# Optimization experiments

Measured on AMD Instinct MI355X. Metric: run time of the kernel, lower is better.

The kernel has to match this reference:

```python
import jax, jax.numpy as jnp
import numpy as np
import math

B, E, H, HD, P, G, N, L, FF = 16, 768, 12, 64, 16, 14, 196, 12, 3072
SQRT_E = math.sqrt(E)
SQRT_HD = math.sqrt(HD)


def cosine_norm(x):
    n = jnp.linalg.norm(x, axis=-1, keepdims=True)
    return x / jnp.maximum(n, 1e-6)


def layer_norm(x, w, b, eps=1e-6):
    m = jnp.mean(x, axis=-1, keepdims=True)
    v = jnp.var(x, axis=-1, keepdims=True)
    return (x - m) / jnp.sqrt(v + eps) * w + b


def setup_inputs() -> dict:
    key = jax.random.key(0)
    ks = jax.random.split(key, 16)
    std = 0.02
    return {
        "x": jax.random.normal(ks[0], (B, 3, 224, 224), jnp.float32),
        "patch_w": jax.random.normal(ks[1], (E, 3, P, P), jnp.float32) * std,
        "patch_b": jnp.zeros((E,), jnp.float32),
        "cls_token": jax.random.normal(ks[2], (1, 1, E), jnp.float32) * std,
        "pos_embed": jax.random.normal(ks[3], (1, N + 1, E), jnp.float32) * std,
        "Wq": jax.random.normal(ks[4], (L, E, E), jnp.float32) * std,
        "Wk": jax.random.normal(ks[5], (L, E, E), jnp.float32) * std,
        "Wv": jax.random.normal(ks[6], (L, E, E), jnp.float32) * std,
        "Wo": jax.random.normal(ks[7], (L, E, E), jnp.float32) * std,
        # Scale params stored at their torch init values (s = ones * scale)
        "s_qk": jnp.ones((L, H, HD), jnp.float32) / SQRT_E,        # scale=1/sqrt(dim)
        "Wup": jax.random.normal(ks[8], (L, FF, E), jnp.float32) * std,
        "Wgate": jax.random.normal(ks[9], (L, FF, E), jnp.float32) * std,
        "Wdown": jax.random.normal(ks[10], (L, E, FF), jnp.float32) * std,
        "s_u": jnp.ones((L, FF), jnp.float32),
        "s_v": jnp.ones((L, FF), jnp.float32),
        "alpha_A": jnp.ones((L, E), jnp.float32) / SQRT_E,         # scale=1/sqrt(dim)
        "alpha_M": jnp.ones((L, E), jnp.float32) / SQRT_E,
        "fc_w": jnp.ones((E,), jnp.float32),
        "fc_b": jnp.zeros((E,), jnp.float32),
    }


def _attention(h, wq, wk, wv, wo, s_qk):
    b, n, _ = h.shape
    q = (h @ wq.T).reshape(b, n, H, HD)
    k = (h @ wk.T).reshape(b, n, H, HD)
    v = (h @ wv.T).reshape(b, n, H, HD)
    # Scale.forward(): s * (init/scale) with init=1, scale=1/sqrt(E)
    s = s_qk * SQRT_E                                   # [H, HD]
    q = cosine_norm(q) * s
    k = cosine_norm(k) * s
    logits = jnp.einsum("bnhd,bmhd->bhnm", q, k) * SQRT_HD
    attn = jax.nn.softmax(logits, axis=-1)
    out = jnp.einsum("bhnm,bmhd->bnhd", attn, v).reshape(b, n, E)
    return out @ wo.T


def _mlp(h, wup, wgate, wdown, s_u, s_v):
    u = (h @ wup.T) * s_u
    v = (h @ wgate.T) * s_v * SQRT_E                    # mlp scale = sqrt(in_features)
    hidden = u * jax.nn.silu(v)
    return hidden @ wdown.T


def _block(h, wq, wk, wv, wo, s_qk, wup, wgate, wdown, s_u, s_v, a_A, a_M):
    # alpha Scale: init=0.05, scale=1/sqrt(E) -> effective = s * 0.05 * sqrt(E)
    aA = a_A * (0.05 * SQRT_E)
    aM = a_M * (0.05 * SQRT_E)
    h_A = cosine_norm(_attention(h, wq, wk, wv, wo, s_qk))
    h = cosine_norm(h + aA * (h_A - h))
    h_M = cosine_norm(_mlp(h, wup, wgate, wdown, s_u, s_v))
    h = cosine_norm(h + aM * (h_M - h))
    return h


def reference(x, patch_w, patch_b, cls_token, pos_embed, Wq, Wk, Wv, Wo, s_qk,
              Wup, Wgate, Wdown, s_u, s_v, alpha_A, alpha_M, fc_w, fc_b):
    b = x.shape[0]
    # patch embed: conv k=stride=16 == patch extraction + linear proj
    patches = x.reshape(b, 3, G, P, G, P).transpose(0, 2, 4, 1, 3, 5).reshape(b, N, 3 * P * P)
    t = patches @ patch_w.reshape(E, -1).T + patch_b    # [B, N, E]
    t = jnp.concatenate([jnp.broadcast_to(cls_token, (b, 1, E)), t], axis=1)
    t = t + pos_embed                                    # [B, N+1, E]
    nodes = None
    for i in range(L):
        t = _block(t, Wq[i], Wk[i], Wv[i], Wo[i], s_qk[i],
                   Wup[i], Wgate[i], Wdown[i], s_u[i], s_v[i], alpha_A[i], alpha_M[i])
        if i == L - 2:
            nodes = layer_norm(t, fc_w, fc_b)[:, 1:]
    edges = layer_norm(t, fc_w, fc_b)[:, 1:]
    return nodes, edges
```

## Files before the change

### kernel.cpp

```cpp
#include <hip/hip_runtime.h>
#include <hip/hip_bf16.h>
#include <cstdint>
#include <cstddef>

typedef __hip_bfloat16 bf16;
typedef short bf16x8 __attribute__((ext_vector_type(8)));
typedef float f32x4 __attribute__((ext_vector_type(4)));

#define SQRT_E   27.712812921102035f
#define ASCALE   (0.05f * 27.712812921102035f)
#define MPAD     3200

__device__ __forceinline__ void load_lds16(const bf16* g, bf16* l) {
    __builtin_amdgcn_global_load_lds(
        (const __attribute__((address_space(1))) void*)g,
        (__attribute__((address_space(3))) void*)l, 16, 0, 0);
}

__device__ __forceinline__ float block_sum(float v, float* sbuf) {
#pragma unroll
    for (int m = 32; m >= 1; m >>= 1) v += __shfl_xor(v, m);
    __syncthreads();
    if ((threadIdx.x & 63) == 0) sbuf[threadIdx.x >> 6] = v;
    __syncthreads();
    return sbuf[0] + sbuf[1] + sbuf[2] + sbuf[3];
}

__device__ __forceinline__ void cvt8(const float* s, bf16* d) {
    float4 f0 = *(const float4*)s;
    float4 f1 = *(const float4*)(s + 4);
    bf16 t[8];
    t[0] = __float2bfloat16(f0.x); t[1] = __float2bfloat16(f0.y);
    t[2] = __float2bfloat16(f0.z); t[3] = __float2bfloat16(f0.w);
    t[4] = __float2bfloat16(f1.x); t[5] = __float2bfloat16(f1.y);
    t[6] = __float2bfloat16(f1.z); t[7] = __float2bfloat16(f1.w);
    *reinterpret_cast<uint4*>(d) = *reinterpret_cast<const uint4*>(t);
}

__device__ __forceinline__ void wconv_body(
    int idx,
    const float* __restrict__ wq, const float* __restrict__ wk,
    const float* __restrict__ wv, const float* __restrict__ wo,
    const float* __restrict__ wu, const float* __restrict__ wg,
    const float* __restrict__ wd, bf16* __restrict__ dst) {
    const float* src;
    size_t off;
    if (idx < 294912) {
        int seg = idx / 73728, o = idx - seg * 73728;
        src = (seg == 0) ? wq : (seg == 1) ? wk : (seg == 2) ? wv : wo;
        off = (size_t)o * 8;
    } else {
        int i2 = idx - 294912;
        int seg = i2 / 294912, o = i2 - seg * 294912;
        src = (seg == 0) ? wu : (seg == 1) ? wg : wd;
        off = (size_t)o * 8;
    }
    cvt8(src + off, dst + (size_t)idx * 8);
}

__global__ __launch_bounds__(256) void prep_kernel(
    const float* __restrict__ x, bf16* __restrict__ A,
    const float* __restrict__ patchw, bf16* __restrict__ pwb,
    const float* __restrict__ wq, const float* __restrict__ wk,
    const float* __restrict__ wv, const float* __restrict__ wo,
    const float* __restrict__ wu, const float* __restrict__ wg,
    const float* __restrict__ wd, bf16* __restrict__ wdst) {
    int b = blockIdx.x, tid = threadIdx.x;
    if (b < 288) {
        int idx = b * 256 + tid;
        cvt8(patchw + (size_t)idx * 8, pwb + (size_t)idx * 8);
    } else if (b < 9888) {
        int idx = (b - 288) * 256 + tid;
        int row = idx / 768, col = idx - row * 768;
        if (row >= 3136) { A[idx] = __float2bfloat16(0.f); return; }
        int bb = row / 196, pp = row - bb * 196;
        int gy = pp / 14, gx = pp - gy * 14;
        int c = col >> 8, rem = col & 255, py = rem >> 4, px = rem & 15;
        A[idx] = __float2bfloat16(
            x[((size_t)(bb * 3 + c) * 224 + gy * 16 + py) * 224 + gx * 16 + px]);
    } else {
        int idx = (b - 9888) * 256 + tid;
        wconv_body(idx, wq, wk, wv, wo, wu, wg, wd, wdst);
    }
}

__global__ __launch_bounds__(256) void assemble_kernel(
    const float* __restrict__ tproj, const float* __restrict__ pb,
    const float* __restrict__ cls, const float* __restrict__ pos,
    float* __restrict__ h, bf16* __restrict__ hb) {
    int row = blockIdx.x;
    int b = row / 197, n = row - b * 197;
#pragma unroll
    for (int i = 0; i < 3; i++) {
        int c = threadIdx.x + i * 256;
        float v;
        if (n == 0) v = cls[c] + pos[c];
        else v = tproj[(size_t)(b * 196 + n - 1) * 768 + c] + pb[c] + pos[(size_t)n * 768 + c];
        h[(size_t)row * 768 + c] = v;
        hb[(size_t)row * 768 + c] = __float2bfloat16(v);
    }
}

__global__ __launch_bounds__(256) void gemm_bt(
    const bf16* __restrict__ A, int lda,
    const bf16* __restrict__ B0, const bf16* __restrict__ B1, const bf16* __restrict__ B2,
    int tilesPerSeg, int segColStride,
    void* __restrict__ Cv, int ldc, long long partStride,
    int Klen, int ldb, int outBf16) {
    __shared__ __align__(16) bf16 As[128 * 32];
    __shared__ __align__(16) bf16 Bs[128 * 32];
    const int tid = threadIdx.x;
    const int lane = tid & 63, wave = tid >> 6;
    const int wm = wave & 1, wn = wave >> 1;
    const int quad = lane >> 4, l16 = lane & 15;
    const int seg = blockIdx.x / tilesPerSeg;
    const int nt = blockIdx.x - seg * tilesPerSeg;
    const bf16* B = (seg == 0) ? B0 : (seg == 1 ? B1 : B2);
    const int row0 = blockIdx.y * 128;
    const int col0 = nt * 128;
    const long long kofs = (long long)blockIdx.z * Klen;
    const bf16* Ab = A + (size_t)row0 * lda + kofs;
    const bf16* Bb = B + (size_t)col0 * ldb + kofs;
    const long long cofs = (long long)blockIdx.z * partStride + (long long)seg * segColStride;

    f32x4 acc[4][4];
    f32x4 zero = {0.f, 0.f, 0.f, 0.f};
#pragma unroll
    for (int i = 0; i < 4; i++)
#pragma unroll
        for (int j = 0; j < 4; j++) acc[i][j] = zero;

    for (int k0 = 0; k0 < Klen; k0 += 32) {
#pragma unroll
        for (int it = 0; it < 2; ++it) {
            int cidx = it * 256 + tid;
            int r = cidx >> 2, cg = cidx & 3;
            load_lds16(Ab + (size_t)r * lda + k0 + cg * 8, As + cidx * 8);
            load_lds16(Bb + (size_t)r * ldb + k0 + cg * 8, Bs + cidx * 8);
        }
        __syncthreads();
        bf16x8 av[4], bv[4];
#pragma unroll
        for (int i = 0; i < 4; i++) {
            av[i] = *(const bf16x8*)(As + (wm * 64 + i * 16 + l16) * 32 + quad * 8);
            bv[i] = *(const bf16x8*)(Bs + (wn * 64 + i * 16 + l16) * 32 + quad * 8);
        }
#pragma unroll
        for (int i = 0; i < 4; i++)
#pragma unroll
            for (int j = 0; j < 4; j++)
                acc[i][j] = __builtin_amdgcn_mfma_f32_16x16x32_bf16(av[i], bv[j], acc[i][j], 0, 0, 0);
        __syncthreads();
    }
    if (outBf16) {
        bf16* Cb = (bf16*)Cv + cofs;
#pragma unroll
        for (int i = 0; i < 4; i++) {
            int rr = row0 + wm * 64 + i * 16 + quad * 4;
#pragma unroll
            for (int j = 0; j < 4; j++) {
                int cc = col0 + wn * 64 + j * 16 + l16;
#pragma unroll
                for (int r = 0; r < 4; r++)
                    Cb[(size_t)(rr + r) * ldc + cc] = __float2bfloat16(acc[i][j][r]);
            }
        }
    } else {
        float* Cb = (float*)Cv + cofs;
#pragma unroll
        for (int i = 0; i < 4; i++) {
            int rr = row0 + wm * 64 + i * 16 + quad * 4;
#pragma unroll
            for (int j = 0; j < 4; j++) {
                int cc = col0 + wn * 64 + j * 16 + l16;
#pragma unroll
                for (int r = 0; r < 4; r++)
                    Cb[(size_t)(rr + r) * ldc + cc] = acc[i][j][r];
            }
        }
    }
}

__global__ __launch_bounds__(256) void oproj_wconv(
    const bf16* __restrict__ A, const bf16* __restrict__ Bw,
    float* __restrict__ C, long long partStride,
    const float* __restrict__ wq, const float* __restrict__ wk,
    const float* __restrict__ wv, const float* __restrict__ wo,
    const float* __restrict__ wu, const float* __restrict__ wg,
    const float* __restrict__ wd, bf16* __restrict__ wdst) {
    __shared__ __align__(16) bf16 As[128 * 32];
    __shared__ __align__(16) bf16 Bs[128 * 32];
    const int bb = blockIdx.x;
    const int tid = threadIdx.x;
    if (bb >= 300) {
        int idx = (bb - 300) * 256 + tid;
        wconv_body(idx, wq, wk, wv, wo, wu, wg, wd, wdst);
        return;
    }
    const int lane = tid & 63, wave = tid >> 6;
    const int wm = wave & 1, wn = wave >> 1;
    const int quad = lane >> 4, l16 = lane & 15;
    const int nt = bb % 6;
    const int ry = (bb / 6) % 25;
    const int z  = bb / 150;
    const int row0 = ry * 128, col0 = nt * 128;
    const bf16* Ab = A + (size_t)row0 * 768 + z * 384;
    const bf16* Bb = Bw + (size_t)col0 * 768 + z * 384;

    f32x4 acc[4][4];
    f32x4 zero = {0.f, 0.f, 0.f, 0.f};
#pragma unroll
    for (int i = 0; i < 4; i++)
#pragma unroll
        for (int j = 0; j < 4; j++) acc[i][j] = zero;

    for (int k0 = 0; k0 < 384; k0 += 32) {
#pragma unroll
        for (int it = 0; it < 2; ++it) {
            int cidx = it * 256 + tid;
            int r = cidx >> 2, cg = cidx & 3;
            load_lds16(Ab + (size_t)r * 768 + k0 + cg * 8, As + cidx * 8);
            load_lds16(Bb + (size_t)r * 768 + k0 + cg * 8, Bs + cidx * 8);
        }
        __syncthreads();
        bf16x8 av[4], bv[4];
#pragma unroll
        for (int i = 0; i < 4; i++) {
            av[i] = *(const bf16x8*)(As + (wm * 64 + i * 16 + l16) * 32 + quad * 8);
            bv[i] = *(const bf16x8*)(Bs + (wn * 64 + i * 16 + l16) * 32 + quad * 8);
        }
#pragma unroll
        for (int i = 0; i < 4; i++)
#pragma unroll
            for (int j = 0; j < 4; j++)
                acc[i][j] = __builtin_amdgcn_mfma_f32_16x16x32_bf16(av[i], bv[j], acc[i][j], 0, 0, 0);
        __syncthreads();
    }
    float* Cb = C + (long long)z * partStride;
#pragma unroll
    for (int i = 0; i < 4; i++) {
        int rr = row0 + wm * 64 + i * 16 + quad * 4;
#pragma unroll
        for (int j = 0; j < 4; j++) {
            int cc = col0 + wn * 64 + j * 16 + l16;
#pragma unroll
            for (int r = 0; r < 4; r++)
                Cb[(size_t)(rr + r) * 768 + cc] = acc[i][j][r];
        }
    }
}

__global__ __launch_bounds__(256) void gemm_qkv(
    const bf16* __restrict__ A,
    const bf16* __restrict__ Bq, const bf16* __restrict__ Bk, const bf16* __restrict__ Bv,
    const float* __restrict__ s_l,
    bf16* __restrict__ Qd, bf16* __restrict__ Kd, bf16* __restrict__ VTd) {
    __shared__ __align__(16) bf16 As[128 * 32];
    __shared__ __align__(16) bf16 Bs[128 * 32];
    const int tid = threadIdx.x;
    const int lane = tid & 63, wave = tid >> 6;
    const int wm = wave & 1, wn = wave >> 1;
    const int quad = lane >> 4, l16 = lane & 15;
    const int seg = blockIdx.x / 6;
    const int nt = blockIdx.x - seg * 6;
    const bf16* B = (seg == 0) ? Bq : (seg == 1 ? Bk : Bv);
    const int row0 = blockIdx.y * 128;
    const int col0 = nt * 128;
    const bf16* Ab = A + (size_t)row0 * 768;
    const bf16* Bb = B + (size_t)col0 * 768;

    f32x4 acc[4][4];
    f32x4 zero = {0.f, 0.f, 0.f, 0.f};
#pragma unroll
    for (int i = 0; i < 4; i++)
#pragma unroll
        for (int j = 0; j < 4; j++) acc[i][j] = zero;

    for (int k0 = 0; k0 < 768; k0 += 32) {
#pragma unroll
        for (int it = 0; it < 2; ++it) {
            int cidx = it * 256 + tid;
            int r = cidx >> 2, cg = cidx & 3;
            load_lds16(Ab + (size_t)r * 768 + k0 + cg * 8, As + cidx * 8);
            load_lds16(Bb + (size_t)r * 768 + k0 + cg * 8, Bs + cidx * 8);
        }
        __syncthreads();
        bf16x8 av[4], bv[4];
#pragma unroll
        for (int i = 0; i < 4; i++) {
            av[i] = *(const bf16x8*)(As + (wm * 64 + i * 16 + l16) * 32 + quad * 8);
            bv[i] = *(const bf16x8*)(Bs + (wn * 64 + i * 16 + l16) * 32 + quad * 8);
        }
#pragma unroll
        for (int i = 0; i < 4; i++)
#pragma unroll
            for (int j = 0; j < 4; j++)
                acc[i][j] = __builtin_amdgcn_mfma_f32_16x16x32_bf16(av[i], bv[j], acc[i][j], 0, 0, 0);
        __syncthreads();
    }

    const int hcol = nt * 2 + wn;
    if (seg < 2) {
        bf16* Dst = (seg == 0) ? Qd : Kd;
        float sv0[4];
#pragma unroll
        for (int j = 0; j < 4; j++) sv0[j] = s_l[hcol * 64 + j * 16 + l16] * SQRT_E;
#pragma unroll
        for (int i = 0; i < 4; i++) {
#pragma unroll
            for (int r = 0; r < 4; r++) {
                float ss = acc[i][0][r] * acc[i][0][r] + acc[i][1][r] * acc[i][1][r]
                         + acc[i][2][r] * acc[i][2][r] + acc[i][3][r] * acc[i][3][r];
#pragma unroll
                for (int m = 1; m < 16; m <<= 1) ss += __shfl_xor(ss, m);
                float inv = 1.f / fmaxf(sqrtf(ss), 1e-6f);
                int t = row0 + wm * 64 + i * 16 + quad * 4 + r;
                if (t < 3152) {
                    int b = t / 197, n = t - b * 197;
                    size_t base = ((size_t)(b * 12 + hcol) * 208 + n) * 64;
#pragma unroll
                    for (int j = 0; j < 4; j++)
                        Dst[base + j * 16 + l16] =
                            __float2bfloat16(acc[i][j][r] * inv * sv0[j]);
                }
            }
        }
    } else {
#pragma unroll
        for (int i = 0; i < 4; i++) {
#pragma unroll
            for (int r = 0; r < 4; r++) {
                int t = row0 + wm * 64 + i * 16 + quad * 4 + r;
                if (t < 3152) {
                    int b = t / 197, n = t - b * 197;
                    size_t vbase = (size_t)(b * 12 + hcol) * 64 * 224 + n;
#pragma unroll
                    for (int j = 0; j < 4; j++)
                        VTd[vbase + (size_t)(j * 16 + l16) * 224] =
                            __float2bfloat16(acc[i][j][r]);
                }
            }
        }
    }
}

__global__ __launch_bounds__(256) void gemm_upgate(
    const bf16* __restrict__ A, const bf16* __restrict__ Bu, const bf16* __restrict__ Bv,
    const float* __restrict__ su, const float* __restrict__ sv,
    bf16* __restrict__ H) {
    __shared__ __align__(16) bf16 As[128 * 32];
    __shared__ __align__(16) bf16 Bus[64 * 32];
    __shared__ __align__(16) bf16 Bvs[64 * 32];
    const int tid = threadIdx.x;
    const int lane = tid & 63, wave = tid >> 6;
    const int wm = wave & 1, wn = wave >> 1;
    const int quad = lane >> 4, l16 = lane & 15;
    const int ct = blockIdx.x;
    const int row0 = blockIdx.y * 128;
    const bf16* Ab = A + (size_t)row0 * 768;
    const bf16* Bub = Bu + (size_t)ct * 64 * 768;
    const bf16* Bvb = Bv + (size_t)ct * 64 * 768;

    f32x4 au[4][2], av_[4][2];
    f32x4 zero = {0.f, 0.f, 0.f, 0.f};
#pragma unroll
    for (int i = 0; i < 4; i++)
#pragma unroll
        for (int j = 0; j < 2; j++) { au[i][j] = zero; av_[i][j] = zero; }

    for (int k0 = 0; k0 < 768; k0 += 32) {
#pragma unroll
        for (int it = 0; it < 2; ++it) {
            int cidx = it * 256 + tid;
            int r = cidx >> 2, cg = cidx & 3;
            load_lds16(Ab + (size_t)r * 768 + k0 + cg * 8, As + cidx * 8);
        }
        {
            int r = tid >> 2, cg = tid & 3;
            load_lds16(Bub + (size_t)r * 768 + k0 + cg * 8, Bus + tid * 8);
            load_lds16(Bvb + (size_t)r * 768 + k0 + cg * 8, Bvs + tid * 8);
        }
        __syncthreads();
        bf16x8 a[4], bu[2], bv[2];
#pragma unroll
        for (int i = 0; i < 4; i++)
            a[i] = *(const bf16x8*)(As + (wm * 64 + i * 16 + l16) * 32 + quad * 8);
#pragma unroll
        for (int j = 0; j < 2; j++) {
            bu[j] = *(const bf16x8*)(Bus + (wn * 32 + j * 16 + l16) * 32 + quad * 8);
            bv[j] = *(const bf16x8*)(Bvs + (wn * 32 + j * 16 + l16) * 32 + quad * 8);
        }
#pragma unroll
        for (int i = 0; i < 4; i++)
#pragma unroll
            for (int j = 0; j < 2; j++) {
                au[i][j]  = __builtin_amdgcn_mfma_f32_16x16x32_bf16(a[i], bu[j], au[i][j], 0, 0, 0);
                av_[i][j] = __builtin_amdgcn_mfma_f32_16x16x32_bf16(a[i], bv[j], av_[i][j], 0, 0, 0);
            }
        __syncthreads();
    }
#pragma unroll
    for (int j = 0; j < 2; j++) {
        int cc = ct * 64 + wn * 32 + j * 16 + l16;
        float suc = su[cc];
        float svc = sv[cc] * SQRT_E;
#pragma unroll
        for (int i = 0; i < 4; i++) {
            int rr = row0 + wm * 64 + i * 16 + quad * 4;
#pragma unroll
            for (int r = 0; r < 4; r++) {
                float u = au[i][j][r] * suc;
                float v = av_[i][j][r] * svc;
                float sig = 1.f / (1.f + __expf(-v));
                H[(size_t)(rr + r) * 3072 + cc] = __float2bfloat16(u * v * sig);
            }
        }
    }
}

__global__ __launch_bounds__(64) void attn_kernel(
    const bf16* __restrict__ Q, const bf16* __restrict__ K,
    const bf16* __restrict__ VT, bf16* __restrict__ O) {
    __shared__ __align__(16) bf16 Ps[16 * 224];
    int lane = threadIdx.x;
    int quad = lane >> 4, l16 = lane & 15;
    int bh = blockIdx.x % 192;
    int qt = blockIdx.x / 192;
    int b = bh / 12, h = bh - b * 12;
    const bf16* Qb = Q + (size_t)bh * 208 * 64;
    const bf16* Kb = K + (size_t)bh * 208 * 64;
    const bf16* Vb = VT + (size_t)bh * 64 * 224;
    f32x4 zero = {0.f, 0.f, 0.f, 0.f};

    bf16x8 a0 = *(const bf16x8*)(Qb + (qt * 16 + l16) * 64 + quad * 8);
    bf16x8 a1 = *(const bf16x8*)(Qb + (qt * 16 + l16) * 64 + quad * 8 + 32);

    f32x4 lg[13];
#pragma unroll
    for (int kt = 0; kt < 13; kt++) {
        bf16x8 b0 = *(const bf16x8*)(Kb + (kt * 16 + l16) * 64 + quad * 8);
        bf16x8 b1 = *(const bf16x8*)(Kb + (kt * 16 + l16) * 64 + quad * 8 + 32);
        f32x4 c = zero;
        c = __builtin_amdgcn_mfma_f32_16x16x32_bf16(a0, b0, c, 0, 0, 0);
        c = __builtin_amdgcn_mfma_f32_16x16x32_bf16(a1, b1, c, 0, 0, 0);
        lg[kt] = c;
    }
    float mx[4] = {-3e38f, -3e38f, -3e38f, -3e38f};
#pragma unroll
    for (int kt = 0; kt < 13; kt++) {
        bool valid = (kt * 16 + l16) < 197;
#pragma unroll
        for (int r = 0; r < 4; r++) {
            float v = valid ? lg[kt][r] * 8.0f : -3e38f;
            lg[kt][r] = v;
            mx[r] = fmaxf(mx[r], v);
        }
    }
#pragma unroll
    for (int m = 1; m < 16; m <<= 1)
#pragma unroll
        for (int r = 0; r < 4; r++) mx[r] = fmaxf(mx[r], __shfl_xor(mx[r], m));
    float sm[4] = {0.f, 0.f, 0.f, 0.f};
#pragma unroll
    for (int kt = 0; kt < 13; kt++)
#pragma unroll
        for (int r = 0; r < 4; r++) {
            float p = __expf(lg[kt][r] - mx[r]);
            lg[kt][r] = p;
            sm[r] += p;
        }
#pragma unroll
    for (int m = 1; m < 16; m <<= 1)
#pragma unroll
        for (int r = 0; r < 4; r++) sm[r] += __shfl_xor(sm[r], m);
    float inv[4];
#pragma unroll
    for (int r = 0; r < 4; r++) inv[r] = 1.f / sm[r];
#pragma unroll
    for (int kt = 0; kt < 13; kt++)
#pragma unroll
        for (int r = 0; r < 4; r++)
            Ps[(quad * 4 + r) * 224 + kt * 16 + l16] = __float2bfloat16(lg[kt][r] * inv[r]);
#pragma unroll
    for (int r = 0; r < 4; r++)
        Ps[(quad * 4 + r) * 224 + 208 + l16] = __float2bfloat16(0.f);
    __syncthreads();
#pragma unroll
    for (int nt = 0; nt < 4; nt++) {
        f32x4 o = zero;
#pragma unroll
        for (int ks = 0; ks < 7; ks++) {
            bf16x8 pa = *(const bf16x8*)(Ps + l16 * 224 + ks * 32 + quad * 8);
            bf16x8 vb = *(const bf16x8*)(Vb + (nt * 16 + l16) * 224 + ks * 32 + quad * 8);
            o = __builtin_amdgcn_mfma_f32_16x16x32_bf16(pa, vb, o, 0, 0, 0);
        }
#pragma unroll
        for (int r = 0; r < 4; r++) {
            int tok = qt * 16 + quad * 4 + r;
            if (tok < 197)
                O[(size_t)(b * 197 + tok) * 768 + h * 64 + nt * 16 + l16] = __float2bfloat16(o[r]);
        }
    }
}

__global__ __launch_bounds__(256) void residual_cos(
    const float* __restrict__ proj, int nParts, long long partStride,
    const float* __restrict__ alpha,
    float* __restrict__ h, bf16* __restrict__ hb) {
    __shared__ float sbuf[4];
    int row = blockIdx.x, tid = threadIdx.x;
    float p[3];
    float ss = 0.f;
#pragma unroll
    for (int i = 0; i < 3; i++) {
        int c = tid + i * 256;
        float v = 0.f;
        for (int pt = 0; pt < nParts; pt++) v += proj[(long long)pt * partStride + (size_t)row * 768 + c];
        p[i] = v;
        ss += v * v;
    }
    ss = block_sum(ss, sbuf);
    float inv1 = 1.f / fmaxf(sqrtf(ss), 1e-6f);
    float ss2 = 0.f;
#pragma unroll
    for (int i = 0; i < 3; i++) {
        int c = tid + i * 256;
        float hv = h[(size_t)row * 768 + c];
        float a = alpha[c] * ASCALE;
        float m = hv + a * (p[i] * inv1 - hv);
        p[i] = m;
        ss2 += m * m;
    }
    ss2 = block_sum(ss2, sbuf);
    float inv2 = 1.f / fmaxf(sqrtf(ss2), 1e-6f);
#pragma unroll
    for (int i = 0; i < 3; i++) {
        int c = tid + i * 256;
        float v = p[i] * inv2;
        h[(size_t)row * 768 + c] = v;
        hb[(size_t)row * 768 + c] = __float2bfloat16(v);
    }
}

__global__ __launch_bounds__(256) void layernorm_out(
    const float* __restrict__ h, const float* __restrict__ w,
    const float* __restrict__ bia, float* __restrict__ out) {
    __shared__ float sbuf[4];
    int bi = blockIdx.x;
    int b = bi / 196, j = bi - b * 196;
    int row = b * 197 + j + 1;
    int tid = threadIdx.x;
    float xv[3];
    float s = 0.f;
#pragma unroll
    for (int i = 0; i < 3; i++) {
        xv[i] = h[(size_t)row * 768 + tid + i * 256];
        s += xv[i];
    }
    s = block_sum(s, sbuf);
    float mean = s * (1.f / 768.f);
    float s2 = 0.f;
#pragma unroll
    for (int i = 0; i < 3; i++) { float d = xv[i] - mean; s2 += d * d; }
    s2 = block_sum(s2, sbuf);
    float var = s2 * (1.f / 768.f);
    float invs = 1.f / sqrtf(var + 1e-6f);
#pragma unroll
    for (int i = 0; i < 3; i++) {
        int c = tid + i * 256;
        out[(size_t)bi * 768 + c] = (xv[i] - mean) * invs * w[c] + bia[c];
    }
}

extern "C" void kernel_launch(void* const* d_in, const int* in_sizes, int n_in,
                              void* d_out, int out_size, void* d_ws, size_t ws_size,
                              hipStream_t stream) {
    (void)in_sizes; (void)n_in; (void)out_size; (void)ws_size;
    const float* x      = (const float*)d_in[0];
    const float* patchw = (const float*)d_in[1];
    const float* patchb = (const float*)d_in[2];
    const float* cls    = (const float*)d_in[3];
    const float* pos    = (const float*)d_in[4];
    const float* Wq     = (const float*)d_in[5];
    const float* Wk     = (const float*)d_in[6];
    const float* Wv     = (const float*)d_in[7];
    const float* Wo     = (const float*)d_in[8];
    const float* s_qk   = (const float*)d_in[9];
    const float* Wup    = (const float*)d_in[10];
    const float* Wgate  = (const float*)d_in[11];
    const float* Wdown  = (const float*)d_in[12];
    const float* s_u    = (const float*)d_in[13];
    const float* s_v    = (const float*)d_in[14];
    const float* alA    = (const float*)d_in[15];
    const float* alM    = (const float*)d_in[16];
    const float* fcw    = (const float*)d_in[17];
    const float* fcb    = (const float*)d_in[18];
    float* out = (float*)d_out;

    char* ws = (char*)d_ws;
    size_t ofs = 0;
    auto alloc = [&](size_t bytes) -> void* {
        void* p = ws + ofs;
        ofs += (bytes + 255) & ~(size_t)255;
        return p;
    };
    float* h      = (float*)alloc((size_t)MPAD * 768 * 4);
    float* part   = (float*)alloc((size_t)4 * MPAD * 768 * 4);
    bf16*  hb     = (bf16*)alloc((size_t)MPAD * 768 * 2);
    bf16*  attno  = (bf16*)alloc((size_t)MPAD * 768 * 2);
    bf16*  hidden = (bf16*)alloc((size_t)MPAD * 3072 * 2);
    size_t qkvt_bytes = ((size_t)192 * 208 * 64 * 2) * 2 + (size_t)192 * 64 * 224 * 2;
    bf16*  Qb     = (bf16*)alloc(qkvt_bytes);
    bf16*  Kb     = Qb + (size_t)192 * 208 * 64;
    bf16*  VTb    = Kb + (size_t)192 * 208 * 64;
    const size_t WPL = 9437184;
    bf16*  wbf0   = (bf16*)alloc(WPL * 2);
    bf16*  wbf1   = (bf16*)alloc(WPL * 2);
    bf16*  pwb    = (bf16*)alloc((size_t)589824 * 2);

    float* tproj  = part;
    bf16*  Apatch = hidden;

    const long long PSTR = (long long)MPAD * 768;
    const size_t EE = 768 * 768, FE = (size_t)3072 * 768;

    prep_kernel<<<14496, 256, 0, stream>>>(x, Apatch, patchw, pwb,
                                           Wq, Wk, Wv, Wo, Wup, Wgate, Wdown, wbf0);
    gemm_bt<<<dim3(6, 25, 1), 256, 0, stream>>>(Apatch, 768, pwb, pwb, pwb,
                                                6, 0, tproj, 768, 0, 768, 768, 0);
    assemble_kernel<<<3152, 256, 0, stream>>>(tproj, patchb, cls, pos, h, hb);
    hipMemsetAsync(Qb, 0, qkvt_bytes, stream);

    for (int l = 0; l < 12; l++) {
        bf16* wl    = (l & 1) ? wbf1 : wbf0;
        bf16* wnext = (l & 1) ? wbf0 : wbf1;
        bf16* wqb = wl;
        bf16* wkb = wl + 589824;
        bf16* wvb = wl + 1179648;
        bf16* wob = wl + 1769472;
        bf16* wub = wl + 2359296;
        bf16* wgb = wl + 4718592;
        bf16* wdb = wl + 7077888;
        int ln = (l < 11) ? (l + 1) : l;

        gemm_qkv<<<dim3(18, 25), 256, 0, stream>>>(hb, wqb, wkb, wvb,
                                                   s_qk + (size_t)l * 768, Qb, Kb, VTb);
        attn_kernel<<<2496, 64, 0, stream>>>(Qb, Kb, VTb, attno);
        oproj_wconv<<<(l < 11) ? 4908 : 300, 256, 0, stream>>>(
            attno, wob, part, PSTR,
            Wq + (size_t)ln * EE, Wk + (size_t)ln * EE,
            Wv + (size_t)ln * EE, Wo + (size_t)ln * EE,
            Wup + (size_t)ln * FE, Wgate + (size_t)ln * FE,
            Wdown + (size_t)ln * FE, wnext);
        residual_cos<<<3152, 256, 0, stream>>>(part, 2, PSTR, alA + (size_t)l * 768, h, hb);
        gemm_upgate<<<dim3(48, 25), 256, 0, stream>>>(hb, wub, wgb,
                                                      s_u + (size_t)l * 3072,
                                                      s_v + (size_t)l * 3072, hidden);
        gemm_bt<<<dim3(6, 25, 4), 256, 0, stream>>>(hidden, 3072, wdb, wdb, wdb,
                                                    6, 0, part, 768, PSTR, 768, 3072, 0);
        residual_cos<<<3152, 256, 0, stream>>>(part, 4, PSTR, alM + (size_t)l * 768, h, hb);

        if (l == 10) layernorm_out<<<3136, 256, 0, stream>>>(h, fcw, fcb, out);
        if (l == 11) layernorm_out<<<3136, 256, 0, stream>>>(h, fcw, fcb, out + 2408448);
    }
}
```

Measured before the change: 2.434 ms.

## Store split-K partials in bf16, drop softmax max pass, fuse layernorm into residual

The O-projection and down-projection partial sums are now written and read as bf16 instead of fp32, which halves the partial-buffer traffic between the GEMMs and residual_cos. The attention softmax skips the max-subtraction pass, since cosine-normalized logits are bounded, and applies the 1/sum normalization to the output instead of to P. The final layernorm is fused into residual_cos, using the unit-norm property to compute variance as 1/768 minus mean squared. In exchange, bf16 partials lose precision in the residual path, and the unstabilized exp relies on the logits staying bounded.

Result: faster. 2.370 ms (-2.6%).

```diff
diff --git a/kernel.cpp b/kernel.cpp
--- a/kernel.cpp
+++ b/kernel.cpp
@@ -183,7 +183,7 @@
 
 __global__ __launch_bounds__(256) void oproj_wconv(
     const bf16* __restrict__ A, const bf16* __restrict__ Bw,
-    float* __restrict__ C, long long partStride,
+    bf16* __restrict__ C, long long partStride,
     const float* __restrict__ wq, const float* __restrict__ wk,
     const float* __restrict__ wv, const float* __restrict__ wo,
     const float* __restrict__ wu, const float* __restrict__ wg,
@@ -236,7 +236,7 @@
                 acc[i][j] = __builtin_amdgcn_mfma_f32_16x16x32_bf16(av[i], bv[j], acc[i][j], 0, 0, 0);
         __syncthreads();
     }
-    float* Cb = C + (long long)z * partStride;
+    bf16* Cb = C + (long long)z * partStride;
 #pragma unroll
     for (int i = 0; i < 4; i++) {
         int rr = row0 + wm * 64 + i * 16 + quad * 4;
@@ -245,7 +245,7 @@
             int cc = col0 + wn * 64 + j * 16 + l16;
 #pragma unroll
             for (int r = 0; r < 4; r++)
-                Cb[(size_t)(rr + r) * 768 + cc] = acc[i][j][r];
+                Cb[(size_t)(rr + r) * 768 + cc] = __float2bfloat16(acc[i][j][r]);
         }
     }
 }
@@ -445,30 +445,17 @@
         c = __builtin_amdgcn_mfma_f32_16x16x32_bf16(a1, b1, c, 0, 0, 0);
         lg[kt] = c;
     }
-    float mx[4] = {-3e38f, -3e38f, -3e38f, -3e38f};
+    float sm[4] = {0.f, 0.f, 0.f, 0.f};
 #pragma unroll
     for (int kt = 0; kt < 13; kt++) {
         bool valid = (kt * 16 + l16) < 197;
 #pragma unroll
         for (int r = 0; r < 4; r++) {
-            float v = valid ? lg[kt][r] * 8.0f : -3e38f;
-            lg[kt][r] = v;
-            mx[r] = fmaxf(mx[r], v);
-        }
-    }
-#pragma unroll
-    for (int m = 1; m < 16; m <<= 1)
-#pragma unroll
-        for (int r = 0; r < 4; r++) mx[r] = fmaxf(mx[r], __shfl_xor(mx[r], m));
-    float sm[4] = {0.f, 0.f, 0.f, 0.f};
-#pragma unroll
-    for (int kt = 0; kt < 13; kt++)
-#pragma unroll
-        for (int r = 0; r < 4; r++) {
-            float p = __expf(lg[kt][r] - mx[r]);
+            float p = valid ? __expf(lg[kt][r] * 8.0f) : 0.f;
             lg[kt][r] = p;
             sm[r] += p;
         }
+    }
 #pragma unroll
     for (int m = 1; m < 16; m <<= 1)
 #pragma unroll
@@ -480,7 +467,7 @@
     for (int kt = 0; kt < 13; kt++)
 #pragma unroll
         for (int r = 0; r < 4; r++)
-            Ps[(quad * 4 + r) * 224 + kt * 16 + l16] = __float2bfloat16(lg[kt][r] * inv[r]);
+            Ps[(quad * 4 + r) * 224 + kt * 16 + l16] = __float2bfloat16(lg[kt][r]);
 #pragma unroll
     for (int r = 0; r < 4; r++)
         Ps[(quad * 4 + r) * 224 + 208 + l16] = __float2bfloat16(0.f);
@@ -498,15 +485,18 @@
         for (int r = 0; r < 4; r++) {
             int tok = qt * 16 + quad * 4 + r;
             if (tok < 197)
-                O[(size_t)(b * 197 + tok) * 768 + h * 64 + nt * 16 + l16] = __float2bfloat16(o[r]);
+                O[(size_t)(b * 197 + tok) * 768 + h * 64 + nt * 16 + l16] =
+                    __float2bfloat16(o[r] * inv[r]);
         }
     }
 }
 
 __global__ __launch_bounds__(256) void residual_cos(
-    const float* __restrict__ proj, int nParts, long long partStride,
+    const bf16* __restrict__ proj, int nParts, long long partStride,
     const float* __restrict__ alpha,
-    float* __restrict__ h, bf16* __restrict__ hb) {
+    float* __restrict__ h, bf16* __restrict__ hb,
+    const float* __restrict__ fcw, const float* __restrict__ fcb,
+    float* __restrict__ lnout) {
     __shared__ float sbuf[4];
     int row = blockIdx.x, tid = threadIdx.x;
     float p[3];
@@ -515,7 +505,8 @@
     for (int i = 0; i < 3; i++) {
         int c = tid + i * 256;
         float v = 0.f;
-        for (int pt = 0; pt < nParts; pt++) v += proj[(long long)pt * partStride + (size_t)row * 768 + c];
+        for (int pt = 0; pt < nParts; pt++)
+            v += __bfloat162float(proj[(long long)pt * partStride + (size_t)row * 768 + c]);
         p[i] = v;
         ss += v * v;
     }
@@ -533,42 +524,28 @@
     }
     ss2 = block_sum(ss2, sbuf);
     float inv2 = 1.f / fmaxf(sqrtf(ss2), 1e-6f);
-#pragma unroll
-    for (int i = 0; i < 3; i++) {
-        int c = tid + i * 256;
-        float v = p[i] * inv2;
-        h[(size_t)row * 768 + c] = v;
-        hb[(size_t)row * 768 + c] = __float2bfloat16(v);
-    }
-}
-
-__global__ __launch_bounds__(256) void layernorm_out(
-    const float* __restrict__ h, const float* __restrict__ w,
-    const float* __restrict__ bia, float* __restrict__ out) {
-    __shared__ float sbuf[4];
-    int bi = blockIdx.x;
-    int b = bi / 196, j = bi - b * 196;
-    int row = b * 197 + j + 1;
-    int tid = threadIdx.x;
-    float xv[3];
-    float s = 0.f;
-#pragma unroll
-    for (int i = 0; i < 3; i++) {
-        xv[i] = h[(size_t)row * 768 + tid + i * 256];
-        s += xv[i];
-    }
-    s = block_sum(s, sbuf);
-    float mean = s * (1.f / 768.f);
-    float s2 = 0.f;
-#pragma unroll
-    for (int i = 0; i < 3; i++) { float d = xv[i] - mean; s2 += d * d; }
-    s2 = block_sum(s2, sbuf);
-    float var = s2 * (1.f / 768.f);
-    float invs = 1.f / sqrtf(var + 1e-6f);
-#pragma unroll
-    for (int i = 0; i < 3; i++) {
-        int c = tid + i * 256;
-        out[(size_t)bi * 768 + c] = (xv[i] - mean) * invs * w[c] + bia[c];
+    float v0 = p[0] * inv2, v1 = p[1] * inv2, v2 = p[2] * inv2;
+    {
+        int c = tid;
+        h[(size_t)row * 768 + c] = v0;
+        hb[(size_t)row * 768 + c] = __float2bfloat16(v0);
+        h[(size_t)row * 768 + c + 256] = v1;
+        hb[(size_t)row * 768 + c + 256] = __float2bfloat16(v1);
+        h[(size_t)row * 768 + c + 512] = v2;
+        hb[(size_t)row * 768 + c + 512] = __float2bfloat16(v2);
+    }
+    if (lnout) {
+        float s = block_sum(v0 + v1 + v2, sbuf);
+        float mean = s * (1.f / 768.f);
+        float var = (1.f / 768.f) - mean * mean;
+        float invs = 1.f / sqrtf(var + 1e-6f);
+        int b = row / 197, n = row - b * 197;
+        if (n >= 1) {
+            size_t obase = (size_t)(b * 196 + n - 1) * 768;
+            lnout[obase + tid]       = (v0 - mean) * invs * fcw[tid] + fcb[tid];
+            lnout[obase + tid + 256] = (v1 - mean) * invs * fcw[tid + 256] + fcb[tid + 256];
+            lnout[obase + tid + 512] = (v2 - mean) * invs * fcw[tid + 512] + fcb[tid + 512];
+        }
     }
 }
 
@@ -619,6 +596,7 @@
     bf16*  pwb    = (bf16*)alloc((size_t)589824 * 2);
 
     float* tproj  = part;
+    bf16*  partb  = (bf16*)part;
     bf16*  Apatch = hidden;
 
     const long long PSTR = (long long)MPAD * 768;
@@ -647,20 +625,20 @@
                                                    s_qk + (size_t)l * 768, Qb, Kb, VTb);
         attn_kernel<<<2496, 64, 0, stream>>>(Qb, Kb, VTb, attno);
         oproj_wconv<<<(l < 11) ? 4908 : 300, 256, 0, stream>>>(
-            attno, wob, part, PSTR,
+            attno, wob, partb, PSTR,
             Wq + (size_t)ln * EE, Wk + (size_t)ln * EE,
             Wv + (size_t)ln * EE, Wo + (size_t)ln * EE,
             Wup + (size_t)ln * FE, Wgate + (size_t)ln * FE,
             Wdown + (size_t)ln * FE, wnext);
-        residual_cos<<<3152, 256, 0, stream>>>(part, 2, PSTR, alA + (size_t)l * 768, h, hb);
+        residual_cos<<<3152, 256, 0, stream>>>(partb, 2, PSTR, alA + (size_t)l * 768,
+                                               h, hb, fcw, fcb, (float*)nullptr);
         gemm_upgate<<<dim3(48, 25), 256, 0, stream>>>(hb, wub, wgb,
                                                       s_u + (size_t)l * 3072,
                                                       s_v + (size_t)l * 3072, hidden);
         gemm_bt<<<dim3(6, 25, 4), 256, 0, stream>>>(hidden, 3072, wdb, wdb, wdb,
-                                                    6, 0, part, 768, PSTR, 768, 3072, 0);
-        residual_cos<<<3152, 256, 0, stream>>>(part, 4, PSTR, alM + (size_t)l * 768, h, hb);
-
-        if (l == 10) layernorm_out<<<3136, 256, 0, stream>>>(h, fcw, fcb, out);
-        if (l == 11) layernorm_out<<<3136, 256, 0, stream>>>(h, fcw, fcb, out + 2408448);
-    }
-}
+                                                    6, 0, partb, 768, PSTR, 768, 3072, 1);
+        float* lnp = (l == 10) ? out : (l == 11) ? (out + 2408448) : (float*)nullptr;
+        residual_cos<<<3152, 256, 0, stream>>>(partb, 4, PSTR, alM + (size_t)l * 768,
+                                               h, hb, fcw, fcb, lnp);
+    }
+}
```
